# Optimization experiments

Measured on AMD Instinct MI355X. Metric: run time of the kernel, lower is better.

The kernel has to match this reference:

```python
import jax, jax.numpy as jnp
import numpy as np

BIG = 1e30  # stand-in for +inf that keeps gradients finite


def setup_inputs() -> dict:
    key = jax.random.key(0)
    B, D, N = 32, 128, 2048
    kx, ky, kl = jax.random.split(key, 3)
    x = jax.random.normal(kx, (B, D, N), dtype=jnp.float32)
    y = jax.random.normal(ky, (B, D, N), dtype=jnp.float32)
    # ragged cardinalities in [N//2, N]; every set nonempty
    lens = jax.random.randint(kl, (B,), N // 2, N + 1)
    mask = jnp.arange(N)[None, :] < lens[:, None]  # [B, N] bool
    return {"x": x, "y": y, "mask": mask}


def reference(x, y, mask):
    # x, y: [B, D, N]; mask: [B, N] bool (shared between x and y, as in original)
    xt = jnp.transpose(x, (0, 2, 1))  # [B, N, D]
    yt = jnp.transpose(y, (0, 2, 1))  # [B, N, D]
    x2 = jnp.sum(xt * xt, axis=-1)    # [B, N]
    y2 = jnp.sum(yt * yt, axis=-1)    # [B, N]
    # pairwise squared L2: [B, N, N], d[b,i,j] = ||x_i - y_j||^2
    d = x2[:, :, None] + y2[:, None, :] - 2.0 * jnp.einsum("bid,bjd->bij", xt, yt)
    m = mask
    # x_dist: for each valid y_j, min over valid x_i; then sum over valid j
    d_row = jnp.where(m[:, :, None], d, BIG)              # mask invalid i
    x_dist = jnp.sum(jnp.where(m, jnp.min(d_row, axis=1), 0.0), axis=1)  # [B]
    # y_dist: for each valid x_i, min over valid y_j; then sum over valid i
    d_col = jnp.where(m[:, None, :], d, BIG)              # mask invalid j
    y_dist = jnp.sum(jnp.where(m, jnp.min(d_col, axis=2), 0.0), axis=1)  # [B]
    return jnp.mean(x_dist + y_dist)
```

## Files before the change

kernel.cpp:

```cpp
#include <hip/hip_runtime.h>
#include <hip/hip_bf16.h>

#define BATCH 32
#define DIM   128
#define NPTS  2048
#define BIGF  1e30f

#define OFF_XT   0ull
#define OFF_YT   16777216ull
#define OFF_XN   33554432ull
#define OFF_YN   (33554432ull + 262144ull)
#define OFF_RMIN (33554432ull + 2ull * 262144ull)
#define OFF_CMIN (33554432ull + 3ull * 262144ull)

typedef __bf16 bf16x8 __attribute__((ext_vector_type(8)));
typedef float  f32x16 __attribute__((ext_vector_type(16)));

#define ZERO16 {0.f,0.f,0.f,0.f,0.f,0.f,0.f,0.f,0.f,0.f,0.f,0.f,0.f,0.f,0.f,0.f}

__device__ __forceinline__ bool mask_is_i32(const void* m) {
  return ((const unsigned char*)m)[1] == 0;
}
__device__ __forceinline__ bool mask_at(const void* m, bool i32, int idx) {
  return i32 ? (((const int*)m)[idx] != 0) : (((const unsigned char*)m)[idx] != 0);
}

__global__ void chamfer_prep(const float* __restrict__ x, const float* __restrict__ y,
                             const void* __restrict__ mask, char* __restrict__ ws,
                             float* __restrict__ out) {
  int blk = blockIdx.x;
  int arr = blk >> 12;
  int b   = (blk >> 7) & 31;
  int pt  = blk & 127;
  int n0  = pt << 4;
  int tid = threadIdx.x;
  int p = tid & 15, c = tid >> 4;

  const float* src = (arr ? y : x) + (size_t)b * DIM * NPTS;
  unsigned short* dstT = (unsigned short*)(ws + (arr ? OFF_YT : OFF_XT))
                         + ((size_t)b * NPTS + n0 + p) * DIM + c * 8;
  float sq = 0.f;
  unsigned short h[8];
#pragma unroll
  for (int q = 0; q < 8; ++q) {
    float v = src[(size_t)(c * 8 + q) * NPTS + n0 + p];
    __hip_bfloat16 bv = __float2bfloat16(v);
    h[q] = *(unsigned short*)&bv;
    float vb = __bfloat162float(bv);
    sq = fmaf(vb, vb, sq);
  }
  uint4 pk;
  pk.x = h[0] | ((unsigned)h[1] << 16);
  pk.y = h[2] | ((unsigned)h[3] << 16);
  pk.z = h[4] | ((unsigned)h[5] << 16);
  pk.w = h[6] | ((unsigned)h[7] << 16);
  *(uint4*)dstT = pk;

  __shared__ float s[256];
  s[tid] = sq;
  __syncthreads();
  if (tid < 16) {
    float tot = 0.f;
#pragma unroll
    for (int cc = 0; cc < 16; ++cc) tot += s[cc * 16 + tid];
    int j = n0 + tid;
    bool i32 = mask_is_i32(mask);
    bool valid = mask_at(mask, i32, b * NPTS + j);
    float nr = valid ? tot : BIGF;
    float* nrm = (float*)(ws + (arr ? OFF_YN : OFF_XN));
    nrm[b * NPTS + j] = nr;
    if (arr) ((unsigned*)(ws + OFF_CMIN))[b * NPTS + j] = __float_as_uint(BIGF);
  }
  if (blk == 0 && tid == 0) out[0] = 0.f;
}

__global__ __launch_bounds__(512, 2)
void chamfer_dist(char* __restrict__ ws) {
  __shared__ unsigned short xs[256 * 128];
  __shared__ unsigned short ys[2][128 * 128];
  __shared__ unsigned colmin_lds[NPTS];

  int blk = blockIdx.x;
  int b  = blk & 31;
  int it = blk >> 5;
  int i0 = it << 8;
  int tid  = threadIdx.x;
  int lane = tid & 63;
  int w    = tid >> 6;
  int qrow = w >> 1, qcol = w & 1;
  int la31 = lane & 31, la5 = lane >> 5;

  const char* xTb = ws + OFF_XT + (size_t)b * NPTS * DIM * 2;
  const char* yTb = ws + OFF_YT + (size_t)b * NPTS * DIM * 2;
  const float* xng = (const float*)(ws + OFF_XN) + b * NPTS;
  const float* yng = (const float*)(ws + OFF_YN) + b * NPTS;
  float*    rowming = (float*)(ws + OFF_RMIN) + b * NPTS;
  unsigned* colming = (unsigned*)(ws + OFF_CMIN) + b * NPTS;

#pragma unroll
  for (int k = 0; k < NPTS / 512; ++k)
    colmin_lds[k * 512 + tid] = __float_as_uint(BIGF);

  char* xsb = (char*)xs;
#pragma unroll
  for (int k = 0; k < 8; ++k) {
    int idx = k * 512 + tid;
    int p = idx >> 4, cc = idx & 15;
    uint4 v = *(const uint4*)(xTb + (size_t)(i0 + p) * 256 + cc * 16);
    *(uint4*)(xsb + p * 256 + ((cc * 16) ^ ((p & 7) << 4))) = v;
  }
  {
    char* dst = (char*)ys[0];
#pragma unroll
    for (int k = 0; k < 4; ++k) {
      int idx = k * 512 + tid;
      int p = idx >> 4, cc = idx & 15;
      uint4 v = *(const uint4*)(yTb + (size_t)p * 256 + cc * 16);
      *(uint4*)(dst + p * 256 + ((cc * 16) ^ ((p & 7) << 4))) = v;
    }
  }

  float xnr[2][16];
#pragma unroll
  for (int fm = 0; fm < 2; ++fm)
#pragma unroll
    for (int r = 0; r < 16; ++r) {
      int row = qrow * 64 + fm * 32 + (r & 3) + ((r >> 2) << 3) + (la5 << 2);
      xnr[fm][r] = xng[i0 + row];
    }
  float rmin[2][16];
#pragma unroll
  for (int fm = 0; fm < 2; ++fm)
#pragma unroll
    for (int r = 0; r < 16; ++r) rmin[fm][r] = BIGF;

  __syncthreads();

  int sx = (la31 & 7) << 4;
  int prow0 = (qrow * 64 + la31) * 256;
  int prow1 = prow0 + 32 * 256;
  int pcol0 = (qcol * 64 + la31) * 256;
  int pcol1 = pcol0 + 32 * 256;

  for (int jt = 0; jt < 16; ++jt) {
    int cur = jt & 1;
    uint4 stg0, stg1, stg2, stg3;
    if (jt < 15) {
      const char* base = yTb + (size_t)(jt + 1) * 128 * 256;
      int i0d = tid, i1d = 512 + tid, i2d = 1024 + tid, i3d = 1536 + tid;
      stg0 = *(const uint4*)(base + (i0d >> 4) * 256 + (i0d & 15) * 16);
      stg1 = *(const uint4*)(base + (i1d >> 4) * 256 + (i1d & 15) * 16);
      stg2 = *(const uint4*)(base + (i2d >> 4) * 256 + (i2d & 15) * 16);
      stg3 = *(const uint4*)(base + (i3d >> 4) * 256 + (i3d & 15) * 16);
    }
    int j0t = jt * 128 + qcol * 64;
    float ynr0 = yng[j0t + la31];
    float ynr1 = yng[j0t + 32 + la31];

    const char* ysb = (const char*)ys[cur];
    f32x16 acc00 = ZERO16, acc01 = ZERO16, acc10 = ZERO16, acc11 = ZERO16;
#pragma unroll
    for (int kc = 0; kc < 8; ++kc) {
      int dbs = (kc * 32 + la5 * 16) ^ sx;
      bf16x8 a0 = *(const bf16x8*)(xsb + prow0 + dbs);
      bf16x8 a1 = *(const bf16x8*)(xsb + prow1 + dbs);
      bf16x8 b0 = *(const bf16x8*)(ysb + pcol0 + dbs);
      bf16x8 b1 = *(const bf16x8*)(ysb + pcol1 + dbs);
      acc00 = __builtin_amdgcn_mfma_f32_32x32x16_bf16(a0, b0, acc00, 0, 0, 0);
      acc01 = __builtin_amdgcn_mfma_f32_32x32x16_bf16(a0, b1, acc01, 0, 0, 0);
      acc10 = __builtin_amdgcn_mfma_f32_32x32x16_bf16(a1, b0, acc10, 0, 0, 0);
      acc11 = __builtin_amdgcn_mfma_f32_32x32x16_bf16(a1, b1, acc11, 0, 0, 0);
    }
    float cm0 = BIGF, cm1 = BIGF;
#pragma unroll
    for (int r = 0; r < 16; ++r) {
      float d;
      d = fmaxf(fmaf(-2.f, acc00[r], xnr[0][r] + ynr0), 0.f);
      rmin[0][r] = fminf(rmin[0][r], d); cm0 = fminf(cm0, d);
      d = fmaxf(fmaf(-2.f, acc01[r], xnr[0][r] + ynr1), 0.f);
      rmin[0][r] = fminf(rmin[0][r], d); cm1 = fminf(cm1, d);
      d = fmaxf(fmaf(-2.f, acc10[r], xnr[1][r] + ynr0), 0.f);
      rmin[1][r] = fminf(rmin[1][r], d); cm0 = fminf(cm0, d);
      d = fmaxf(fmaf(-2.f, acc11[r], xnr[1][r] + ynr1), 0.f);
      rmin[1][r] = fminf(rmin[1][r], d); cm1 = fminf(cm1, d);
    }
    cm0 = fminf(cm0, __shfl_xor(cm0, 32));
    cm1 = fminf(cm1, __shfl_xor(cm1, 32));
    if (lane < 32) {
      atomicMin(&colmin_lds[jt * 128 + qcol * 64 + la31],      __float_as_uint(cm0));
      atomicMin(&colmin_lds[jt * 128 + qcol * 64 + 32 + la31], __float_as_uint(cm1));
    }
    if (jt < 15) {
      char* dst = (char*)ys[cur ^ 1];
      int i0d = tid, i1d = 512 + tid, i2d = 1024 + tid, i3d = 1536 + tid;
      *(uint4*)(dst + (i0d >> 4) * 256 + (((i0d & 15) * 16) ^ (((i0d >> 4) & 7) << 4))) = stg0;
      *(uint4*)(dst + (i1d >> 4) * 256 + (((i1d & 15) * 16) ^ (((i1d >> 4) & 7) << 4))) = stg1;
      *(uint4*)(dst + (i2d >> 4) * 256 + (((i2d & 15) * 16) ^ (((i2d >> 4) & 7) << 4))) = stg2;
      *(uint4*)(dst + (i3d >> 4) * 256 + (((i3d & 15) * 16) ^ (((i3d >> 4) & 7) << 4))) = stg3;
    }
    __syncthreads();
  }

  for (int idx = tid; idx < NPTS; idx += 512)
    atomicMin(&colming[idx], colmin_lds[idx]);

#pragma unroll
  for (int fm = 0; fm < 2; ++fm)
#pragma unroll
    for (int r = 0; r < 16; ++r) {
      float v = rmin[fm][r];
      v = fminf(v, __shfl_xor(v, 1));
      v = fminf(v, __shfl_xor(v, 2));
      v = fminf(v, __shfl_xor(v, 4));
      v = fminf(v, __shfl_xor(v, 8));
      v = fminf(v, __shfl_xor(v, 16));
      if (la31 == 0) {
        int row = qrow * 64 + fm * 32 + (r & 3) + ((r >> 2) << 3) + (la5 << 2);
        rowming[i0 + row] = v;
      }
    }
}

__global__ void chamfer_reduce(const char* __restrict__ ws, const void* __restrict__ mask,
                               float* __restrict__ out) {
  __shared__ float red[256];
  int b = blockIdx.x;
  int tid = threadIdx.x;
  bool i32 = mask_is_i32(mask);
  const float*    rowmin = (const float*)(ws + OFF_RMIN) + b * NPTS;
  const unsigned* colmin = (const unsigned*)(ws + OFF_CMIN) + b * NPTS;
  float s = 0.f;
  for (int i = tid; i < NPTS; i += 256) {
    if (mask_at(mask, i32, b * NPTS + i))
      s += rowmin[i] + __uint_as_float(colmin[i]);
  }
  red[tid] = s;
  __syncthreads();
  for (int st = 128; st > 0; st >>= 1) {
    if (tid < st) red[tid] += red[tid + st];
    __syncthreads();
  }
  if (tid == 0) atomicAdd(out, red[0] * (1.f / BATCH));
}

extern "C" void kernel_launch(void* const* d_in, const int* in_sizes, int n_in,
                              void* d_out, int out_size, void* d_ws, size_t ws_size,
                              hipStream_t stream) {
  const float* x = (const float*)d_in[0];
  const float* y = (const float*)d_in[1];
  const void* mask = d_in[2];
  float* out = (float*)d_out;
  char* ws = (char*)d_ws;

  chamfer_prep<<<8192, 256, 0, stream>>>(x, y, mask, ws, out);
  chamfer_dist<<<256, 512, 0, stream>>>(ws);
  chamfer_reduce<<<32, 256, 0, stream>>>(ws, mask, out);
}
```

Baseline: 162.4 us.

## Tile prep transpose through LDS, pre-swizzle bf16 layout, keep X fragments in registers

```diff
diff --git a/kernel.cpp b/kernel.cpp
--- a/kernel.cpp
+++ b/kernel.cpp
@@ -28,55 +28,66 @@
 __global__ void chamfer_prep(const float* __restrict__ x, const float* __restrict__ y,
                              const void* __restrict__ mask, char* __restrict__ ws,
                              float* __restrict__ out) {
+  __shared__ float buf[128 * 132];
+  __shared__ float nrm_part[2][128];
+
   int blk = blockIdx.x;
-  int arr = blk >> 12;
-  int b   = (blk >> 7) & 31;
-  int pt  = blk & 127;
-  int n0  = pt << 4;
+  int arr = blk >> 9;
+  int b   = (blk >> 4) & 31;
+  int nt  = blk & 15;
+  int n0  = nt << 7;
   int tid = threadIdx.x;
-  int p = tid & 15, c = tid >> 4;
 
   const float* src = (arr ? y : x) + (size_t)b * DIM * NPTS;
-  unsigned short* dstT = (unsigned short*)(ws + (arr ? OFF_YT : OFF_XT))
-                         + ((size_t)b * NPTS + n0 + p) * DIM + c * 8;
+
+#pragma unroll
+  for (int k = 0; k < 16; ++k) {
+    int idx = k * 256 + tid;
+    int d = idx >> 5, c4 = idx & 31;
+    float4 v = *(const float4*)(src + (size_t)d * NPTS + n0 + c4 * 4);
+    *(float4*)&buf[d * 132 + c4 * 4] = v;
+  }
+  __syncthreads();
+
+  int n = tid & 127, half = tid >> 7;
+  char* img = ws + (arr ? OFF_YT : OFF_XT) + ((size_t)b * NPTS + n0 + n) * 256;
   float sq = 0.f;
-  unsigned short h[8];
-#pragma unroll
-  for (int q = 0; q < 8; ++q) {
-    float v = src[(size_t)(c * 8 + q) * NPTS + n0 + p];
-    __hip_bfloat16 bv = __float2bfloat16(v);
-    h[q] = *(unsigned short*)&bv;
-    float vb = __bfloat162float(bv);
-    sq = fmaf(vb, vb, sq);
-  }
-  uint4 pk;
-  pk.x = h[0] | ((unsigned)h[1] << 16);
-  pk.y = h[2] | ((unsigned)h[3] << 16);
-  pk.z = h[4] | ((unsigned)h[5] << 16);
-  pk.w = h[6] | ((unsigned)h[7] << 16);
-  *(uint4*)dstT = pk;
-
-  __shared__ float s[256];
-  s[tid] = sq;
-  __syncthreads();
-  if (tid < 16) {
-    float tot = 0.f;
-#pragma unroll
-    for (int cc = 0; cc < 16; ++cc) tot += s[cc * 16 + tid];
-    int j = n0 + tid;
+#pragma unroll
+  for (int cl = 0; cl < 8; ++cl) {
+    unsigned short h[8];
+#pragma unroll
+    for (int q = 0; q < 8; ++q) {
+      int d = half * 64 + cl * 8 + q;
+      float v = buf[d * 132 + n];
+      __hip_bfloat16 bv = __float2bfloat16(v);
+      h[q] = *(unsigned short*)&bv;
+      float vb = __bfloat162float(bv);
+      sq = fmaf(vb, vb, sq);
+    }
+    uint4 pk;
+    pk.x = h[0] | ((unsigned)h[1] << 16);
+    pk.y = h[2] | ((unsigned)h[3] << 16);
+    pk.z = h[4] | ((unsigned)h[5] << 16);
+    pk.w = h[6] | ((unsigned)h[7] << 16);
+    int cg = half * 8 + cl;
+    *(uint4*)(img + ((cg ^ (n & 7)) << 4)) = pk;
+  }
+  nrm_part[half][n] = sq;
+  __syncthreads();
+  if (half == 0) {
+    float tot = nrm_part[0][n] + nrm_part[1][n];
+    int row = n0 + n;
     bool i32 = mask_is_i32(mask);
-    bool valid = mask_at(mask, i32, b * NPTS + j);
-    float nr = valid ? tot : BIGF;
+    bool valid = mask_at(mask, i32, b * NPTS + row);
     float* nrm = (float*)(ws + (arr ? OFF_YN : OFF_XN));
-    nrm[b * NPTS + j] = nr;
-    if (arr) ((unsigned*)(ws + OFF_CMIN))[b * NPTS + j] = __float_as_uint(BIGF);
+    nrm[b * NPTS + row] = valid ? tot : BIGF;
+    if (arr) ((unsigned*)(ws + OFF_CMIN))[b * NPTS + row] = __float_as_uint(BIGF);
   }
   if (blk == 0 && tid == 0) out[0] = 0.f;
 }
 
 __global__ __launch_bounds__(512, 2)
 void chamfer_dist(char* __restrict__ ws) {
-  __shared__ unsigned short xs[256 * 128];
   __shared__ unsigned short ys[2][128 * 128];
   __shared__ unsigned colmin_lds[NPTS];
 
@@ -90,8 +101,8 @@
   int qrow = w >> 1, qcol = w & 1;
   int la31 = lane & 31, la5 = lane >> 5;
 
-  const char* xTb = ws + OFF_XT + (size_t)b * NPTS * DIM * 2;
-  const char* yTb = ws + OFF_YT + (size_t)b * NPTS * DIM * 2;
+  const char* xTb = ws + OFF_XT + (size_t)b * NPTS * 256;
+  const char* yTb = ws + OFF_YT + (size_t)b * NPTS * 256;
   const float* xng = (const float*)(ws + OFF_XN) + b * NPTS;
   const float* yng = (const float*)(ws + OFF_YN) + b * NPTS;
   float*    rowming = (float*)(ws + OFF_RMIN) + b * NPTS;
@@ -101,23 +112,16 @@
   for (int k = 0; k < NPTS / 512; ++k)
     colmin_lds[k * 512 + tid] = __float_as_uint(BIGF);
 
-  char* xsb = (char*)xs;
-#pragma unroll
-  for (int k = 0; k < 8; ++k) {
-    int idx = k * 512 + tid;
-    int p = idx >> 4, cc = idx & 15;
-    uint4 v = *(const uint4*)(xTb + (size_t)(i0 + p) * 256 + cc * 16);
-    *(uint4*)(xsb + p * 256 + ((cc * 16) ^ ((p & 7) << 4))) = v;
-  }
-  {
-    char* dst = (char*)ys[0];
-#pragma unroll
-    for (int k = 0; k < 4; ++k) {
-      int idx = k * 512 + tid;
-      int p = idx >> 4, cc = idx & 15;
-      uint4 v = *(const uint4*)(yTb + (size_t)p * 256 + cc * 16);
-      *(uint4*)(dst + p * 256 + ((cc * 16) ^ ((p & 7) << 4))) = v;
-    }
+  int r0 = i0 + qrow * 64 + la31;
+  int swA = (la31 & 7) << 4;
+  const char* xrow0 = xTb + (size_t)r0 * 256;
+  const char* xrow1 = xrow0 + 32 * 256;
+  bf16x8 Areg0[8], Areg1[8];
+#pragma unroll
+  for (int kc = 0; kc < 8; ++kc) {
+    int dbs = (((kc * 2 + la5) << 4)) ^ swA;
+    Areg0[kc] = *(const bf16x8*)(xrow0 + dbs);
+    Areg1[kc] = *(const bf16x8*)(xrow1 + dbs);
   }
 
   float xnr[2][16];
@@ -134,11 +138,14 @@
 #pragma unroll
     for (int r = 0; r < 16; ++r) rmin[fm][r] = BIGF;
 
-  __syncthreads();
-
-  int sx = (la31 & 7) << 4;
-  int prow0 = (qrow * 64 + la31) * 256;
-  int prow1 = prow0 + 32 * 256;
+#pragma unroll
+  for (int k = 0; k < 4; ++k) {
+    int idx = k * 512 + tid;
+    *(uint4*)((char*)ys[0] + idx * 16) = *(const uint4*)(yTb + (size_t)idx * 16);
+  }
+  __syncthreads();
+
+  int sw = (la31 & 7) << 4;
   int pcol0 = (qcol * 64 + la31) * 256;
   int pcol1 = pcol0 + 32 * 256;
 
@@ -147,11 +154,10 @@
     uint4 stg0, stg1, stg2, stg3;
     if (jt < 15) {
       const char* base = yTb + (size_t)(jt + 1) * 128 * 256;
-      int i0d = tid, i1d = 512 + tid, i2d = 1024 + tid, i3d = 1536 + tid;
-      stg0 = *(const uint4*)(base + (i0d >> 4) * 256 + (i0d & 15) * 16);
-      stg1 = *(const uint4*)(base + (i1d >> 4) * 256 + (i1d & 15) * 16);
-      stg2 = *(const uint4*)(base + (i2d >> 4) * 256 + (i2d & 15) * 16);
-      stg3 = *(const uint4*)(base + (i3d >> 4) * 256 + (i3d & 15) * 16);
+      stg0 = *(const uint4*)(base + (size_t)(tid)        * 16);
+      stg1 = *(const uint4*)(base + (size_t)(512  + tid) * 16);
+      stg2 = *(const uint4*)(base + (size_t)(1024 + tid) * 16);
+      stg3 = *(const uint4*)(base + (size_t)(1536 + tid) * 16);
     }
     int j0t = jt * 128 + qcol * 64;
     float ynr0 = yng[j0t + la31];
@@ -161,15 +167,13 @@
     f32x16 acc00 = ZERO16, acc01 = ZERO16, acc10 = ZERO16, acc11 = ZERO16;
 #pragma unroll
     for (int kc = 0; kc < 8; ++kc) {
-      int dbs = (kc * 32 + la5 * 16) ^ sx;
-      bf16x8 a0 = *(const bf16x8*)(xsb + prow0 + dbs);
-      bf16x8 a1 = *(const bf16x8*)(xsb + prow1 + dbs);
+      int dbs = ((kc * 2 + la5) << 4) ^ sw;
       bf16x8 b0 = *(const bf16x8*)(ysb + pcol0 + dbs);
       bf16x8 b1 = *(const bf16x8*)(ysb + pcol1 + dbs);
-      acc00 = __builtin_amdgcn_mfma_f32_32x32x16_bf16(a0, b0, acc00, 0, 0, 0);
-      acc01 = __builtin_amdgcn_mfma_f32_32x32x16_bf16(a0, b1, acc01, 0, 0, 0);
-      acc10 = __builtin_amdgcn_mfma_f32_32x32x16_bf16(a1, b0, acc10, 0, 0, 0);
-      acc11 = __builtin_amdgcn_mfma_f32_32x32x16_bf16(a1, b1, acc11, 0, 0, 0);
+      acc00 = __builtin_amdgcn_mfma_f32_32x32x16_bf16(Areg0[kc], b0, acc00, 0, 0, 0);
+      acc01 = __builtin_amdgcn_mfma_f32_32x32x16_bf16(Areg0[kc], b1, acc01, 0, 0, 0);
+      acc10 = __builtin_amdgcn_mfma_f32_32x32x16_bf16(Areg1[kc], b0, acc10, 0, 0, 0);
+      acc11 = __builtin_amdgcn_mfma_f32_32x32x16_bf16(Areg1[kc], b1, acc11, 0, 0, 0);
     }
     float cm0 = BIGF, cm1 = BIGF;
 #pragma unroll
@@ -187,16 +191,15 @@
     cm0 = fminf(cm0, __shfl_xor(cm0, 32));
     cm1 = fminf(cm1, __shfl_xor(cm1, 32));
     if (lane < 32) {
-      atomicMin(&colmin_lds[jt * 128 + qcol * 64 + la31],      __float_as_uint(cm0));
-      atomicMin(&colmin_lds[jt * 128 + qcol * 64 + 32 + la31], __float_as_uint(cm1));
+      atomicMin(&colmin_lds[j0t + la31],      __float_as_uint(cm0));
+      atomicMin(&colmin_lds[j0t + 32 + la31], __float_as_uint(cm1));
     }
     if (jt < 15) {
       char* dst = (char*)ys[cur ^ 1];
-      int i0d = tid, i1d = 512 + tid, i2d = 1024 + tid, i3d = 1536 + tid;
-      *(uint4*)(dst + (i0d >> 4) * 256 + (((i0d & 15) * 16) ^ (((i0d >> 4) & 7) << 4))) = stg0;
-      *(uint4*)(dst + (i1d >> 4) * 256 + (((i1d & 15) * 16) ^ (((i1d >> 4) & 7) << 4))) = stg1;
-      *(uint4*)(dst + (i2d >> 4) * 256 + (((i2d & 15) * 16) ^ (((i2d >> 4) & 7) << 4))) = stg2;
-      *(uint4*)(dst + (i3d >> 4) * 256 + (((i3d & 15) * 16) ^ (((i3d >> 4) & 7) << 4))) = stg3;
+      *(uint4*)(dst + (size_t)(tid)        * 16) = stg0;
+      *(uint4*)(dst + (size_t)(512  + tid) * 16) = stg1;
+      *(uint4*)(dst + (size_t)(1024 + tid) * 16) = stg2;
+      *(uint4*)(dst + (size_t)(1536 + tid) * 16) = stg3;
     }
     __syncthreads();
   }
@@ -252,7 +255,7 @@
   float* out = (float*)d_out;
   char* ws = (char*)d_ws;
 
-  chamfer_prep<<<8192, 256, 0, stream>>>(x, y, mask, ws, out);
+  chamfer_prep<<<1024, 256, 0, stream>>>(x, y, mask, ws, out);
   chamfer_dist<<<256, 512, 0, stream>>>(ws);
   chamfer_reduce<<<32, 256, 0, stream>>>(ws, mask, out);
 }
```

Measured after the change: 159.2 us. No clear change (-2.0%).
